# Kernel optimization log

Measured on AMD Instinct MI355X. Metric: run time of the kernel, lower is better.

Reference implementation:

```python
import jax, jax.numpy as jnp
import numpy as np
from jax import lax

B, S, TW = 16, 128, 16
VOCAB, EDIM = 50000, 300
NCHARS, CEDIM, CH = 100, 50, 50
HID = 256
NTAGS, MAXR = 10, 16
H2 = 2 * HID


def _lstm_dir(x, mask, wih, whh, b):
    # x: [N,T,D], mask: [N,T] bool. Returns masked outputs [N,T,H] and final hidden [N,H].
    Hd = whh.shape[1]
    Nn = x.shape[0]

    def step(carry, inp):
        h, c = carry
        xt, m = inp  # xt [N,D], m [N,1]
        z = xt @ wih.T + h @ whh.T + b
        i, f, g, o = jnp.split(z, 4, axis=-1)
        c_new = jax.nn.sigmoid(f) * c + jax.nn.sigmoid(i) * jnp.tanh(g)
        h_new = jax.nn.sigmoid(o) * jnp.tanh(c_new)
        c = jnp.where(m, c_new, c)
        h = jnp.where(m, h_new, h)
        return (h, c), jnp.where(m, h_new, 0.0)

    h0 = jnp.zeros((Nn, Hd), x.dtype)
    (hn, _), ys = lax.scan(step, (h0, h0), (x.transpose(1, 0, 2), mask.T[..., None]))
    return ys.transpose(1, 0, 2), hn


def _bilstm(x, lengths, pf, pb):
    # Mirrors pack_padded_sequence -> LSTM -> pad_packed (zeros past length).
    T = x.shape[1]
    mask = jnp.arange(T)[None, :] < lengths[:, None]
    yf, hf = _lstm_dir(x, mask, *pf)
    # per-sequence reversal for the backward direction
    idx = jnp.maximum(lengths[:, None] - 1 - jnp.arange(T)[None, :], 0)
    xr = jnp.take_along_axis(x, idx[:, :, None], axis=1)
    ybr, hb = _lstm_dir(xr, mask, *pb)
    yb = jnp.take_along_axis(ybr, idx[:, :, None], axis=1) * mask[:, :, None]
    return jnp.concatenate([yf, yb], -1), jnp.concatenate([hf, hb], -1)


def _forward(emb, char_emb, c_wih_f, c_whh_f, c_b_f, c_wih_b, c_whh_b, c_b_b,
             w_wih_f, w_whh_f, w_b_f, w_wih_b, w_whh_b, w_b_b, clf_w, clf_b,
             sentences, sentence_lengths, word_chars, word_lengths):
    word_repr = emb[sentences]  # [B,S,EDIM]
    # CharLSTM: final bi-hidden per word (all words of all sentences batched)
    cw = word_chars.reshape(B * S, TW)
    cl = word_lengths.reshape(B * S)
    ce = char_emb[cw]  # [B*S,TW,CEDIM]
    _, hn = _bilstm(ce, cl, (c_wih_f, c_whh_f, c_b_f), (c_wih_b, c_whh_b, c_b_b))
    sent_mask = jnp.arange(S)[None, :] < sentence_lengths[:, None]
    char_feat = hn.reshape(B, S, 2 * CH) * sent_mask[:, :, None]  # pad_sequence zeros
    x = jnp.concatenate([word_repr, char_feat], -1)  # [B,S,400]
    out, _ = _bilstm(x, sentence_lengths, (w_wih_f, w_whh_f, w_b_f), (w_wih_b, w_whh_b, w_b_b))
    u = out.transpose(1, 0, 2)  # [S,B,2H]  (unpacked.transpose(0,1))
    # prefix sums collapse the exhaustive sliding-window means into one pass
    csum = jnp.concatenate([jnp.zeros((1, B, H2), u.dtype), jnp.cumsum(u, axis=0)], 0)
    starts = np.concatenate([np.arange(0, S - r + 1) for r in range(1, MAXR + 1)])
    sizes = np.concatenate([np.full(S - r + 1, r) for r in range(1, MAXR + 1)])
    first = u[starts]                                   # [N,B,2H]
    last = u[starts + sizes - 1]                        # [N,B,2H]
    mean = (csum[starts + sizes] - csum[starts]) / jnp.asarray(sizes, u.dtype)[:, None, None]
    feats = jnp.concatenate([first, mean, last], -1)    # [N,B,6H]
    logits = jax.nn.relu(feats) @ clf_w.T + clf_b       # [N,B,NTAGS]
    return logits.transpose(1, 2, 0)                    # [B,NTAGS,N] (stack dim=-1)


def setup_inputs() -> dict:
    key = jax.random.key(0)
    ks = jax.random.split(key, 12)
    sc = 0.08

    def lstm_p(k, D, Hd):
        k1, k2, k3 = jax.random.split(k, 3)
        return (jax.random.normal(k1, (4 * Hd, D), jnp.float32) * sc,
                jax.random.normal(k2, (4 * Hd, Hd), jnp.float32) * sc,
                jax.random.normal(k3, (4 * Hd,), jnp.float32) * sc)

    emb = (jax.random.normal(ks[0], (VOCAB, EDIM), jnp.float32) * sc).at[0].set(0.0)
    char_emb = (jax.random.normal(ks[1], (NCHARS, CEDIM), jnp.float32) * sc).at[0].set(0.0)
    c_wih_f, c_whh_f, c_b_f = lstm_p(ks[2], CEDIM, CH)
    c_wih_b, c_whh_b, c_b_b = lstm_p(ks[3], CEDIM, CH)
    w_wih_f, w_whh_f, w_b_f = lstm_p(ks[4], EDIM + 2 * CH, HID)
    w_wih_b, w_whh_b, w_b_b = lstm_p(ks[5], EDIM + 2 * CH, HID)
    clf_w = jax.random.normal(ks[6], (NTAGS, 3 * H2), jnp.float32) * sc
    clf_b = jax.random.normal(ks[7], (NTAGS,), jnp.float32) * sc

    sentences = jax.random.randint(ks[8], (B, S), 1, VOCAB, jnp.int32)
    sl = jnp.sort(jax.random.randint(ks[9], (B,), S // 2, S + 1, jnp.int32))[::-1]
    sentence_lengths = sl.at[0].set(S)  # descending; max_len = S (static)
    word_chars = jax.random.randint(ks[10], (B, S, TW), 1, NCHARS, jnp.int32)
    word_lengths = jax.random.randint(ks[11], (B, S), 1, TW + 1, jnp.int32)

    return dict(emb=emb, char_emb=char_emb,
                c_wih_f=c_wih_f, c_whh_f=c_whh_f, c_b_f=c_b_f,
                c_wih_b=c_wih_b, c_whh_b=c_whh_b, c_b_b=c_b_b,
                w_wih_f=w_wih_f, w_whh_f=w_whh_f, w_b_f=w_b_f,
                w_wih_b=w_wih_b, w_whh_b=w_whh_b, w_b_b=w_b_b,
                clf_w=clf_w, clf_b=clf_b,
                sentences=sentences, sentence_lengths=sentence_lengths,
                word_chars=word_chars, word_lengths=word_lengths)


def reference(emb, char_emb, c_wih_f, c_whh_f, c_b_f, c_wih_b, c_whh_b, c_b_b,
              w_wih_f, w_whh_f, w_b_f, w_wih_b, w_whh_b, w_b_b, clf_w, clf_b,
              sentences, sentence_lengths, word_chars, word_lengths):
    return _forward(emb, char_emb, c_wih_f, c_whh_f, c_b_f, c_wih_b, c_whh_b, c_b_b,
                    w_wih_f, w_whh_f, w_b_f, w_wih_b, w_whh_b, w_b_b, clf_w, clf_b,
                    sentences, sentence_lengths, word_chars, word_lengths)
```

## Files before the change

kernel.cpp:

```cpp
#include <hip/hip_runtime.h>
#include <math.h>

typedef unsigned int u32;
typedef unsigned short u16;
typedef __attribute__((ext_vector_type(8))) short short8;
typedef __attribute__((ext_vector_type(4))) float f32x4;
typedef __attribute__((ext_vector_type(4))) u32 u32x4;

#define NB 16
#define NS 128
#define NTW 16
#define NEDIM 300
#define NCED 50
#define NCH 50
#define NTAGS 10
#define XDIM 400
#define NWIN 1928

__device__ __forceinline__ float sigf(float x){ return 1.0f/(1.0f+__expf(-x)); }
__device__ __forceinline__ float tanhfast(float x){
  float e = __expf(2.0f*x);
  return 1.0f - 2.0f/(e + 1.0f);
}
__device__ __forceinline__ u16 f2bu(float f){
  u32 u = __float_as_uint(f);
  return (u16)((u + 0x7fffu + ((u>>16)&1u))>>16);
}
__device__ __forceinline__ float bf2f(u16 x){ return __uint_as_float(((u32)x)<<16); }

__global__ void k_embed(const float* __restrict__ emb, const int* __restrict__ sent,
                        float* __restrict__ x){
  int n = blockIdx.x;
  int row = sent[n];
  const float* src = emb + (size_t)row*NEDIM;
  float* dst = x + (size_t)n*XDIM;
  for (int d = threadIdx.x; d < NEDIM; d += blockDim.x) dst[d] = src[d];
}

__global__ void k_char(const float* __restrict__ char_emb,
                       const float* __restrict__ wih_f, const float* __restrict__ whh_f, const float* __restrict__ b_f,
                       const float* __restrict__ wih_b, const float* __restrict__ whh_b, const float* __restrict__ b_b,
                       const int* __restrict__ wchars, const int* __restrict__ wlens,
                       const int* __restrict__ slens, float* __restrict__ x){
  const int dir = blockIdx.y;
  const int tid = threadIdx.x;
  __shared__ u16 wih_l[200*NCED];
  __shared__ u16 whh_l[200*NCED];
  __shared__ float z_l[200];
  __shared__ float h_l[NCH];
  const float* wih = dir ? wih_b : wih_f;
  const float* whh = dir ? whh_b : whh_f;
  const float* bp  = dir ? b_b   : b_f;
  for (int i = tid; i < 200*NCED; i += 256){
    wih_l[i] = f2bu(wih[i]);
    whh_l[i] = f2bu(whh[i]);
  }
  float bias = (tid < 200) ? bp[tid] : 0.f;
  __syncthreads();
  for (int w = 0; w < 4; ++w){
    int n = blockIdx.x*4 + w;
    int b = n >> 7, s = n & 127;
    int len = wlens[n];
    float c = 0.f, hcur = 0.f;
    if (tid < NCH) h_l[tid] = 0.f;
    __syncthreads();
    for (int t = 0; t < len; ++t){
      int tt = dir ? (len-1-t) : t;
      int ch = wchars[n*NTW + tt];
      if (tid < 200){
        const float* xe = char_emb + ch*NCED;
        const u16* wr = wih_l + tid*NCED;
        const u16* ur = whh_l + tid*NCED;
        float acc = bias;
        #pragma unroll 10
        for (int k = 0; k < NCED; ++k){
          float wv = __uint_as_float(((u32)wr[k])<<16);
          float uv = __uint_as_float(((u32)ur[k])<<16);
          acc += wv*xe[k] + uv*h_l[k];
        }
        z_l[tid] = acc;
      }
      __syncthreads();
      if (tid < NCH){
        float gi = sigf(z_l[tid]);
        float gf = sigf(z_l[NCH+tid]);
        float gg = tanhf(z_l[2*NCH+tid]);
        float go = sigf(z_l[3*NCH+tid]);
        c = gf*c + gi*gg;
        hcur = go*tanhf(c);
        h_l[tid] = hcur;
      }
      __syncthreads();
    }
    if (tid < NCH){
      float v = (s < slens[b]) ? hcur : 0.f;
      x[(size_t)n*XDIM + NEDIM + dir*NCH + tid] = v;
    }
  }
}

__global__ void k_wxg(const float* __restrict__ x,
                      const float* __restrict__ wih_f, const float* __restrict__ wih_b,
                      const float* __restrict__ bw_f, const float* __restrict__ bw_b,
                      u16* __restrict__ xgb){
  __shared__ float As[16][65];
  __shared__ float Bs[16][65];
  int tid = threadIdx.x;
  int tx = tid & 15, ty = tid >> 4;
  int n0 = blockIdx.x * 64;
  int m0 = blockIdx.y * 64;
  int dir = n0 >> 10;
  int j0  = n0 & 1023;
  const float* wih = dir ? wih_b : wih_f;
  const float* bw  = dir ? bw_b  : bw_f;
  float acc[4][4] = {};
  for (int k0 = 0; k0 < 400; k0 += 16){
    #pragma unroll
    for (int i = 0; i < 4; ++i){
      int e = tid + i*256;
      int kk = e & 15, m = e >> 4;
      As[kk][m] = x[(m0+m)*XDIM + k0 + kk];
      Bs[kk][m] = wih[(j0+m)*XDIM + k0 + kk];
    }
    __syncthreads();
    #pragma unroll
    for (int kk = 0; kk < 16; ++kk){
      float av[4], bv[4];
      #pragma unroll
      for (int i=0;i<4;++i) av[i] = As[kk][ty*4+i];
      #pragma unroll
      for (int j=0;j<4;++j) bv[j] = Bs[kk][tx*4+j];
      #pragma unroll
      for (int i=0;i<4;++i)
        #pragma unroll
        for (int j=0;j<4;++j) acc[i][j] = fmaf(av[i], bv[j], acc[i][j]);
    }
    __syncthreads();
  }
  #pragma unroll
  for (int i=0;i<4;++i){
    int m = m0 + ty*4 + i;
    #pragma unroll
    for (int j=0;j<4;++j){
      int jj = j0 + tx*4 + j;
      xgb[(size_t)dir*2097152 + m*1024 + jj] = f2bu(acc[i][j] + bw[jj]);
    }
  }
}

__global__ __launch_bounds__(1024, 4) void k_wlstm2(
    const float* __restrict__ whh_f, const float* __restrict__ whh_b,
    const u16* __restrict__ xgB, const int* __restrict__ slens,
    float* __restrict__ out, u32* __restrict__ xh, int* __restrict__ flags){
  const int dir  = blockIdx.x >> 1;
  const int half = blockIdx.x & 1;
  const int tid  = threadIdx.x;
  const int lane = tid & 63;
  const int w    = tid >> 6;
  const int q    = lane >> 4;
  const int jc   = lane & 15;

  __shared__ __align__(16) u16  Hbuf[2][16*256];
  __shared__ __align__(16) float abuf[32][64][4];
  __shared__ __align__(16) u16  xstg[2][16*512];

  const float* whh = dir ? whh_b : whh_f;

  const int v = w & 7, rsel = w >> 3;
  const int b0c = q*4 + 2*rsel, b1c = b0c + 1;
  const int len0 = slens[b0c], len1 = slens[b1c];
  const int len_s = slens[w];

  short8 Bf[2][8];
  #pragma unroll
  for (int l = 0; l < 2; ++l){
    int jt = w*2 + l;
    int g = jt >> 3, vv = jt & 7;
    int j = g*256 + half*128 + vv*16 + jc;
    const float* wr = whh + (size_t)j*256;
    #pragma unroll
    for (int kc = 0; kc < 8; ++kc){
      int k0 = kc*32 + q*8;
      f32x4 w0 = *(const f32x4*)(wr + k0);
      f32x4 w1 = *(const f32x4*)(wr + k0 + 4);
      short8 s;
      s[0]=(short)f2bu(w0[0]); s[1]=(short)f2bu(w0[1]);
      s[2]=(short)f2bu(w0[2]); s[3]=(short)f2bu(w0[3]);
      s[4]=(short)f2bu(w1[0]); s[5]=(short)f2bu(w1[1]);
      s[6]=(short)f2bu(w1[2]); s[7]=(short)f2bu(w1[3]);
      Bf[l][kc] = s;
    }
  }

  for (int i = tid; i < 2048; i += 1024) ((u32*)Hbuf[0])[i] = 0u;

  {
    int rowS = dir ? (len_s - 1) : 0;
    const u16* src = xgB + ((size_t)dir<<21) + ((w*128 + rowS)*1024 + q*256 + half*128 + jc*8);
    u32x4 d = *(const u32x4*)src;
    *(u32x4*)&xstg[0][(w*4 + q)*128 + jc*8] = d;
  }
  __syncthreads();

  const int fl_idx = dir*2 + half;
  const int fl_p   = dir*2 + (1 - half);
  u32* xh_own = xh + fl_idx*2048;
  u32* xh_par = xh + fl_p*2048;

  float c0 = 0.f, c1 = 0.f, h0 = 0.f, h1 = 0.f;
  int cur = 0;

  for (int t = 0; t < 128; ++t){
    u32x4 stg;
    const bool do_stage = (t < 127);
    if (do_stage){
      int rowS = dir ? (len_s - 2 - t) : (t + 1);
      rowS = rowS < 0 ? 0 : rowS;
      const u16* src = xgB + ((size_t)dir<<21) + ((w*128 + rowS)*1024 + q*256 + half*128 + jc*8);
      stg = *(const u32x4*)src;
    }

    f32x4 acc0 = {0.f,0.f,0.f,0.f};
    f32x4 acc1 = {0.f,0.f,0.f,0.f};
    {
      const char* Hc = (const char*)Hbuf[cur];
      int arow = jc;
      #pragma unroll
      for (int kc = 0; kc < 8; ++kc){
        int kb = (kc*64 + q*16) ^ ((arow & 7) << 4);
        short8 af = *(const short8*)(Hc + arow*512 + kb);
        acc0 = __builtin_amdgcn_mfma_f32_16x16x32_bf16(af, Bf[0][kc], acc0, 0, 0, 0);
        acc1 = __builtin_amdgcn_mfma_f32_16x16x32_bf16(af, Bf[1][kc], acc1, 0, 0, 0);
      }
    }
    *(f32x4*)&abuf[w*2  ][lane][0] = acc0;
    *(f32x4*)&abuf[w*2+1][lane][0] = acc1;
    __syncthreads();

    int nxt = cur ^ 1;
    {
      f32x4 zi = *(const f32x4*)&abuf[0*8+v][lane][0];
      f32x4 zf = *(const f32x4*)&abuf[1*8+v][lane][0];
      f32x4 zg = *(const f32x4*)&abuf[2*8+v][lane][0];
      f32x4 zo = *(const f32x4*)&abuf[3*8+v][lane][0];
      const u16* xs = xstg[t & 1];
      const int ucol = v*16 + jc;
      const int ug   = half*128 + ucol;

      float Zi0 = (rsel ? zi[2] : zi[0]) + bf2f(xs[(b0c*4+0)*128 + ucol]);
      float Zf0 = (rsel ? zf[2] : zf[0]) + bf2f(xs[(b0c*4+1)*128 + ucol]);
      float Zg0 = (rsel ? zg[2] : zg[0]) + bf2f(xs[(b0c*4+2)*128 + ucol]);
      float Zo0 = (rsel ? zo[2] : zo[0]) + bf2f(xs[(b0c*4+3)*128 + ucol]);
      if (t < len0){
        float gi = sigf(Zi0), gf = sigf(Zf0), gg = tanhfast(Zg0), go = sigf(Zo0);
        c0 = gf*c0 + gi*gg;
        h0 = go*tanhfast(c0);
        int row = dir ? (len0-1-t) : t;
        out[((b0c<<7)+row)*512 + dir*256 + ug] = h0;
      }
      float Zi1 = (rsel ? zi[3] : zi[1]) + bf2f(xs[(b1c*4+0)*128 + ucol]);
      float Zf1 = (rsel ? zf[3] : zf[1]) + bf2f(xs[(b1c*4+1)*128 + ucol]);
      float Zg1 = (rsel ? zg[3] : zg[1]) + bf2f(xs[(b1c*4+2)*128 + ucol]);
      float Zo1 = (rsel ? zo[3] : zo[1]) + bf2f(xs[(b1c*4+3)*128 + ucol]);
      if (t < len1){
        float gi = sigf(Zi1), gf = sigf(Zf1), gg = tanhfast(Zg1), go = sigf(Zo1);
        c1 = gf*c1 + gi*gg;
        h1 = go*tanhfast(c1);
        int row = dir ? (len1-1-t) : t;
        out[((b1c<<7)+row)*512 + dir*256 + ug] = h1;
      }
      u16 hb0 = f2bu(h0), hb1 = f2bu(h1);
      Hbuf[nxt][b0c*256 + ((((ug*2) ^ ((b0c&7)<<4))) >> 1)] = hb0;
      Hbuf[nxt][b1c*256 + ((((ug*2) ^ ((b1c&7)<<4))) >> 1)] = hb1;
      u32 pack = ((u32)hb1 << 16) | (u32)hb0;
      __hip_atomic_store(&xh_own[(t&1)*1024 + ucol*8 + q*2 + rsel], pack,
                         __ATOMIC_RELAXED, __HIP_MEMORY_SCOPE_AGENT);
    }
    __syncthreads();

    if (tid == 0){
      __hip_atomic_store(&flags[fl_idx], t+1, __ATOMIC_RELEASE, __HIP_MEMORY_SCOPE_AGENT);
      int spins = 0;
      while (__hip_atomic_load(&flags[fl_p], __ATOMIC_ACQUIRE, __HIP_MEMORY_SCOPE_AGENT) < t+1){
        __builtin_amdgcn_s_sleep(2);
        if (++spins > (1<<16)) break;
      }
    }
    __syncthreads();

    {
      u32 d = __hip_atomic_load(&xh_par[(t&1)*1024 + tid],
                                __ATOMIC_RELAXED, __HIP_MEMORY_SCOPE_AGENT);
      int ul  = tid >> 3;
      int qq  = (tid >> 1) & 3, rs = tid & 1;
      int bb0 = qq*4 + rs*2, bb1 = bb0 + 1;
      int ugp = (1-half)*128 + ul;
      Hbuf[nxt][bb0*256 + ((((ugp*2) ^ ((bb0&7)<<4))) >> 1)] = (u16)(d & 0xffffu);
      Hbuf[nxt][bb1*256 + ((((ugp*2) ^ ((bb1&7)<<4))) >> 1)] = (u16)(d >> 16);
    }
    if (do_stage){
      *(u32x4*)&xstg[(t+1)&1][(w*4 + q)*128 + jc*8] = stg;
    }
    __syncthreads();
    cur = nxt;
  }
}

__global__ void k_csum(const float* __restrict__ out, float* __restrict__ csum){
  int gid = blockIdx.x*256 + threadIdx.x;
  int b = gid >> 9, d = gid & 511;
  float run = 0.f;
  csum[(b*129)*512 + d] = 0.f;
  for (int s = 0; s < 128; ++s){
    run += out[((b<<7)+s)*512 + d];
    csum[(b*129 + s + 1)*512 + d] = run;
  }
}

__global__ void k_ac(const float* __restrict__ out, const float* __restrict__ clf_w,
                     float* __restrict__ A, float* __restrict__ Cm){
  int gid = blockIdx.x*256 + threadIdx.x;
  int bs = gid / 10, tag = gid % 10;
  const float* o  = out + bs*512;
  const float* w1 = clf_w + tag*1536;
  const float* w3 = w1 + 1024;
  float a=0.f, cc=0.f;
  for (int d = 0; d < 512; ++d){
    float vv = fmaxf(o[d], 0.f);
    a  = fmaf(vv, w1[d], a);
    cc = fmaf(vv, w3[d], cc);
  }
  A[gid] = a; Cm[gid] = cc;
}

__global__ void k_clf(const float* __restrict__ csum, const float* __restrict__ clf_w,
                      const float* __restrict__ clf_b, const float* __restrict__ A,
                      const float* __restrict__ Cm, float* __restrict__ dout){
  __shared__ float w2_l[NTAGS*512];
  int tid = threadIdx.x;
  for (int i = tid; i < NTAGS*512; i += 256){
    int tag = i >> 9, d = i & 511;
    w2_l[i] = clf_w[tag*1536 + 512 + d];
  }
  __syncthreads();
  int qq = blockIdx.x*4 + (tid >> 6);
  int lane = tid & 63;
  int n = qq >> 4, b = qq & 15;
  int rem = n, r = 1;
  while (rem >= 129 - r){ rem -= 129 - r; ++r; }
  int s0 = rem, s1 = s0 + r - 1;
  float invr = 1.0f / (float)r;
  int d0 = lane*8;
  const float* c0 = csum + (b*129 + s0    )*512 + d0;
  const float* c1 = csum + (b*129 + s0 + r)*512 + d0;
  float m[8];
  #pragma unroll
  for (int i=0;i<8;++i) m[i] = fmaxf((c1[i]-c0[i])*invr, 0.f);
  float p[10];
  #pragma unroll
  for (int tag=0; tag<NTAGS; ++tag){
    const float* wv = w2_l + tag*512 + d0;
    float s = 0.f;
    #pragma unroll
    for (int i=0;i<8;++i) s = fmaf(m[i], wv[i], s);
    #pragma unroll
    for (int off=32; off>=1; off>>=1) s += __shfl_xor(s, off);
    p[tag] = s;
  }
  if (lane == 0){
    #pragma unroll
    for (int tag=0; tag<NTAGS; ++tag){
      float vv = p[tag] + A[(b*128+s0)*10+tag] + Cm[(b*128+s1)*10+tag] + clf_b[tag];
      dout[b*(NTAGS*NWIN) + tag*NWIN + n] = vv;
    }
  }
}

extern "C" void kernel_launch(void* const* d_in, const int* in_sizes, int n_in,
                              void* d_out, int out_size, void* d_ws, size_t ws_size,
                              hipStream_t stream){
  (void)in_sizes; (void)n_in; (void)out_size; (void)ws_size;
  const float* emb      = (const float*)d_in[0];
  const float* char_emb = (const float*)d_in[1];
  const float* c_wih_f  = (const float*)d_in[2];
  const float* c_whh_f  = (const float*)d_in[3];
  const float* c_b_f    = (const float*)d_in[4];
  const float* c_wih_b  = (const float*)d_in[5];
  const float* c_whh_b  = (const float*)d_in[6];
  const float* c_b_b    = (const float*)d_in[7];
  const float* w_wih_f  = (const float*)d_in[8];
  const float* w_whh_f  = (const float*)d_in[9];
  const float* w_b_f    = (const float*)d_in[10];
  const float* w_wih_b  = (const float*)d_in[11];
  const float* w_whh_b  = (const float*)d_in[12];
  const float* w_b_b    = (const float*)d_in[13];
  const float* clf_w    = (const float*)d_in[14];
  const float* clf_b    = (const float*)d_in[15];
  const int* sentences  = (const int*)d_in[16];
  const int* slens      = (const int*)d_in[17];
  const int* wchars     = (const int*)d_in[18];
  const int* wlens      = (const int*)d_in[19];

  float* ws   = (float*)d_ws;
  float* x    = ws;
  u16*  xgb   = (u16*)(ws + 819200);
  float* outb = ws + 2916352;
  float* csum = ws + 3964928;
  float* A    = ws + 5021696;
  float* Cm   = ws + 5042176;
  u32*  xh    = (u32*)(ws + 5062656);
  int*  flags = (int*)(ws + 5070848);

  hipMemsetAsync(outb, 0, (size_t)2048*512*sizeof(float), stream);
  hipMemsetAsync(flags, 0, 256, stream);
  k_embed<<<2048, 256, 0, stream>>>(emb, sentences, x);
  k_char<<<dim3(512,2), 256, 0, stream>>>(char_emb, c_wih_f, c_whh_f, c_b_f,
                                          c_wih_b, c_whh_b, c_b_b,
                                          wchars, wlens, slens, x);
  k_wxg<<<dim3(32,32), 256, 0, stream>>>(x, w_wih_f, w_wih_b, w_b_f, w_b_b, xgb);
  k_wlstm2<<<4, 1024, 0, stream>>>(w_whh_f, w_whh_b, xgb, slens, outb, xh, flags);
  k_csum<<<32, 256, 0, stream>>>(outb, csum);
  k_ac<<<80, 256, 0, stream>>>(outb, clf_w, A, Cm);
  k_clf<<<7712, 256, 0, stream>>>(csum, clf_w, clf_b, A, Cm, (float*)d_out);
}
```

Measured before the change: 899.3 us.

## Run each word-LSTM direction in one block, removing cross-block flag sync

The word-level recurrent kernel now uses a single 512-thread block per direction instead of two cooperating 1024-thread blocks. Those blocks exchanged half of the hidden state through global atomics and spin flags every timestep; that exchange is gone. Recurrent weights are split between registers (first 6 k-tiles) and LDS (last 2), and the input-gate projection is written by the GEMM kernel in a time-major layout already permuted per thread, so each step does four contiguous vector loads. The cost is twice the MFMA work per block and fewer threads per direction on the serial critical path.

```diff
diff --git a/kernel.cpp b/kernel.cpp
--- a/kernel.cpp
+++ b/kernel.cpp
@@ -102,7 +102,8 @@
 __global__ void k_wxg(const float* __restrict__ x,
                       const float* __restrict__ wih_f, const float* __restrict__ wih_b,
                       const float* __restrict__ bw_f, const float* __restrict__ bw_b,
-                      u16* __restrict__ xgb){
+                      const int* __restrict__ slens,
+                      u16* __restrict__ xgT){
   __shared__ float As[16][65];
   __shared__ float Bs[16][65];
   int tid = threadIdx.x;
@@ -137,169 +138,157 @@
     }
     __syncthreads();
   }
+  int b_ = m0 >> 7;
+  int len = slens[b_];
+  int q_ = b_ >> 2, r_ = b_ & 3;
   #pragma unroll
   for (int i=0;i<4;++i){
     int m = m0 + ty*4 + i;
-    #pragma unroll
-    for (int j=0;j<4;++j){
-      int jj = j0 + tx*4 + j;
-      xgb[(size_t)dir*2097152 + m*1024 + jj] = f2bu(acc[i][j] + bw[jj]);
-    }
-  }
-}
-
-__global__ __launch_bounds__(1024, 4) void k_wlstm2(
+    int row = m & 127;
+    int t = dir ? (len-1-row) : row;
+    if (t >= 0){
+      #pragma unroll
+      for (int j=0;j<4;++j){
+        int jj = j0 + tx*4 + j;
+        float v = acc[i][j] + bw[jj];
+        int g = jj >> 8, u = jj & 255;
+        int ut = u >> 4, jc_ = u & 15;
+        int w_ = ut >> 1, u2_ = ut & 1;
+        int p_ = g & 1, gg_ = g >> 1;
+        int tid_ = w_*64 + q_*16 + jc_;
+        size_t e = ((size_t)((dir<<7) + t)*512 + tid_)*32 + p_*16 + gg_*8 + u2_*4 + r_;
+        xgT[e] = f2bu(v);
+      }
+    }
+  }
+}
+
+__global__ __launch_bounds__(512, 2) void k_wlstm3(
     const float* __restrict__ whh_f, const float* __restrict__ whh_b,
-    const u16* __restrict__ xgB, const int* __restrict__ slens,
-    float* __restrict__ out, u32* __restrict__ xh, int* __restrict__ flags){
-  const int dir  = blockIdx.x >> 1;
-  const int half = blockIdx.x & 1;
+    const u16* __restrict__ xgT, const int* __restrict__ slens,
+    float* __restrict__ out){
+  const int dir  = blockIdx.x;
   const int tid  = threadIdx.x;
   const int lane = tid & 63;
   const int w    = tid >> 6;
   const int q    = lane >> 4;
   const int jc   = lane & 15;
 
-  __shared__ __align__(16) u16  Hbuf[2][16*256];
-  __shared__ __align__(16) float abuf[32][64][4];
-  __shared__ __align__(16) u16  xstg[2][16*512];
+  __shared__ __align__(16) u32 WL[2][64][64][4];
+  __shared__ __align__(16) u16 Hs[2][16][256];
 
   const float* whh = dir ? whh_b : whh_f;
 
-  const int v = w & 7, rsel = w >> 3;
-  const int b0c = q*4 + 2*rsel, b1c = b0c + 1;
-  const int len0 = slens[b0c], len1 = slens[b1c];
-  const int len_s = slens[w];
-
-  short8 Bf[2][8];
+  int lenr[4];
   #pragma unroll
-  for (int l = 0; l < 2; ++l){
-    int jt = w*2 + l;
-    int g = jt >> 3, vv = jt & 7;
-    int j = g*256 + half*128 + vv*16 + jc;
-    const float* wr = whh + (size_t)j*256;
-    #pragma unroll
-    for (int kc = 0; kc < 8; ++kc){
-      int k0 = kc*32 + q*8;
-      f32x4 w0 = *(const f32x4*)(wr + k0);
-      f32x4 w1 = *(const f32x4*)(wr + k0 + 4);
-      short8 s;
-      s[0]=(short)f2bu(w0[0]); s[1]=(short)f2bu(w0[1]);
-      s[2]=(short)f2bu(w0[2]); s[3]=(short)f2bu(w0[3]);
-      s[4]=(short)f2bu(w1[0]); s[5]=(short)f2bu(w1[1]);
-      s[6]=(short)f2bu(w1[2]); s[7]=(short)f2bu(w1[3]);
-      Bf[l][kc] = s;
-    }
-  }
-
-  for (int i = tid; i < 2048; i += 1024) ((u32*)Hbuf[0])[i] = 0u;
-
-  {
-    int rowS = dir ? (len_s - 1) : 0;
-    const u16* src = xgB + ((size_t)dir<<21) + ((w*128 + rowS)*1024 + q*256 + half*128 + jc*8);
-    u32x4 d = *(const u32x4*)src;
-    *(u32x4*)&xstg[0][(w*4 + q)*128 + jc*8] = d;
-  }
+  for (int r=0;r<4;++r) lenr[r] = slens[q*4+r];
+
+  short8 Wf[4][2][6];
+  #pragma unroll
+  for (int g=0; g<4; ++g){
+    #pragma unroll
+    for (int u2=0; u2<2; ++u2){
+      int j = g*256 + (2*w+u2)*16 + jc;
+      const float* wr = whh + (size_t)j*256;
+      #pragma unroll
+      for (int kt=0; kt<6; ++kt){
+        int k0 = kt*32 + q*8;
+        f32x4 w0 = *(const f32x4*)(wr + k0);
+        f32x4 w1 = *(const f32x4*)(wr + k0 + 4);
+        short8 s;
+        s[0]=(short)f2bu(w0[0]); s[1]=(short)f2bu(w0[1]);
+        s[2]=(short)f2bu(w0[2]); s[3]=(short)f2bu(w0[3]);
+        s[4]=(short)f2bu(w1[0]); s[5]=(short)f2bu(w1[1]);
+        s[6]=(short)f2bu(w1[2]); s[7]=(short)f2bu(w1[3]);
+        Wf[g][u2][kt] = s;
+      }
+    }
+  }
+
+  for (int idx = tid; idx < 2*64*64; idx += 512){
+    int kt2 = idx >> 12; int rem = idx & 4095;
+    int jt = rem >> 6;   int ln = rem & 63;
+    int g = jt >> 4, ut = jt & 15;
+    int j = g*256 + ut*16 + (ln & 15);
+    int k0 = (6+kt2)*32 + (ln>>4)*8;
+    const float* wr = whh + (size_t)j*256 + k0;
+    f32x4 w0 = *(const f32x4*)(wr);
+    f32x4 w1 = *(const f32x4*)(wr + 4);
+    WL[kt2][jt][ln][0] = ((u32)f2bu(w0[1])<<16) | f2bu(w0[0]);
+    WL[kt2][jt][ln][1] = ((u32)f2bu(w0[3])<<16) | f2bu(w0[2]);
+    WL[kt2][jt][ln][2] = ((u32)f2bu(w1[1])<<16) | f2bu(w1[0]);
+    WL[kt2][jt][ln][3] = ((u32)f2bu(w1[3])<<16) | f2bu(w1[2]);
+  }
+
+  for (int i = tid; i < 2048; i += 512) ((u32*)Hs[0])[i] = 0u;
   __syncthreads();
 
-  const int fl_idx = dir*2 + half;
-  const int fl_p   = dir*2 + (1 - half);
-  u32* xh_own = xh + fl_idx*2048;
-  u32* xh_par = xh + fl_p*2048;
-
-  float c0 = 0.f, c1 = 0.f, h0 = 0.f, h1 = 0.f;
+  float c[2][4] = {{0.f,0.f,0.f,0.f},{0.f,0.f,0.f,0.f}};
+  float P[2][4];
+  const u16* xbase = xgT + ((size_t)(dir*128)*512 + tid)*32;
   int cur = 0;
 
   for (int t = 0; t < 128; ++t){
-    u32x4 stg;
-    const bool do_stage = (t < 127);
-    if (do_stage){
-      int rowS = dir ? (len_s - 2 - t) : (t + 1);
-      rowS = rowS < 0 ? 0 : rowS;
-      const u16* src = xgB + ((size_t)dir<<21) + ((w*128 + rowS)*1024 + q*256 + half*128 + jc*8);
-      stg = *(const u32x4*)src;
-    }
-
-    f32x4 acc0 = {0.f,0.f,0.f,0.f};
-    f32x4 acc1 = {0.f,0.f,0.f,0.f};
-    {
-      const char* Hc = (const char*)Hbuf[cur];
-      int arow = jc;
-      #pragma unroll
-      for (int kc = 0; kc < 8; ++kc){
-        int kb = (kc*64 + q*16) ^ ((arow & 7) << 4);
-        short8 af = *(const short8*)(Hc + arow*512 + kb);
-        acc0 = __builtin_amdgcn_mfma_f32_16x16x32_bf16(af, Bf[0][kc], acc0, 0, 0, 0);
-        acc1 = __builtin_amdgcn_mfma_f32_16x16x32_bf16(af, Bf[1][kc], acc1, 0, 0, 0);
-      }
-    }
-    *(f32x4*)&abuf[w*2  ][lane][0] = acc0;
-    *(f32x4*)&abuf[w*2+1][lane][0] = acc1;
-    __syncthreads();
-
+    const u16* xp = xbase + (size_t)t*16384;
+    u32x4 xv[4];
+    #pragma unroll
+    for (int i=0;i<4;++i) xv[i] = *(const u32x4*)(xp + i*8);
+
+    const char* Hc = (const char*)Hs[cur];
     int nxt = cur ^ 1;
-    {
-      f32x4 zi = *(const f32x4*)&abuf[0*8+v][lane][0];
-      f32x4 zf = *(const f32x4*)&abuf[1*8+v][lane][0];
-      f32x4 zg = *(const f32x4*)&abuf[2*8+v][lane][0];
-      f32x4 zo = *(const f32x4*)&abuf[3*8+v][lane][0];
-      const u16* xs = xstg[t & 1];
-      const int ucol = v*16 + jc;
-      const int ug   = half*128 + ucol;
-
-      float Zi0 = (rsel ? zi[2] : zi[0]) + bf2f(xs[(b0c*4+0)*128 + ucol]);
-      float Zf0 = (rsel ? zf[2] : zf[0]) + bf2f(xs[(b0c*4+1)*128 + ucol]);
-      float Zg0 = (rsel ? zg[2] : zg[0]) + bf2f(xs[(b0c*4+2)*128 + ucol]);
-      float Zo0 = (rsel ? zo[2] : zo[0]) + bf2f(xs[(b0c*4+3)*128 + ucol]);
-      if (t < len0){
-        float gi = sigf(Zi0), gf = sigf(Zf0), gg = tanhfast(Zg0), go = sigf(Zo0);
-        c0 = gf*c0 + gi*gg;
-        h0 = go*tanhfast(c0);
-        int row = dir ? (len0-1-t) : t;
-        out[((b0c<<7)+row)*512 + dir*256 + ug] = h0;
-      }
-      float Zi1 = (rsel ? zi[3] : zi[1]) + bf2f(xs[(b1c*4+0)*128 + ucol]);
-      float Zf1 = (rsel ? zf[3] : zf[1]) + bf2f(xs[(b1c*4+1)*128 + ucol]);
-      float Zg1 = (rsel ? zg[3] : zg[1]) + bf2f(xs[(b1c*4+2)*128 + ucol]);
-      float Zo1 = (rsel ? zo[3] : zo[1]) + bf2f(xs[(b1c*4+3)*128 + ucol]);
-      if (t < len1){
-        float gi = sigf(Zi1), gf = sigf(Zf1), gg = tanhfast(Zg1), go = sigf(Zo1);
-        c1 = gf*c1 + gi*gg;
-        h1 = go*tanhfast(c1);
-        int row = dir ? (len1-1-t) : t;
-        out[((b1c<<7)+row)*512 + dir*256 + ug] = h1;
-      }
-      u16 hb0 = f2bu(h0), hb1 = f2bu(h1);
-      Hbuf[nxt][b0c*256 + ((((ug*2) ^ ((b0c&7)<<4))) >> 1)] = hb0;
-      Hbuf[nxt][b1c*256 + ((((ug*2) ^ ((b1c&7)<<4))) >> 1)] = hb1;
-      u32 pack = ((u32)hb1 << 16) | (u32)hb0;
-      __hip_atomic_store(&xh_own[(t&1)*1024 + ucol*8 + q*2 + rsel], pack,
-                         __ATOMIC_RELAXED, __HIP_MEMORY_SCOPE_AGENT);
-    }
-    __syncthreads();
-
-    if (tid == 0){
-      __hip_atomic_store(&flags[fl_idx], t+1, __ATOMIC_RELEASE, __HIP_MEMORY_SCOPE_AGENT);
-      int spins = 0;
-      while (__hip_atomic_load(&flags[fl_p], __ATOMIC_ACQUIRE, __HIP_MEMORY_SCOPE_AGENT) < t+1){
-        __builtin_amdgcn_s_sleep(2);
-        if (++spins > (1<<16)) break;
-      }
-    }
-    __syncthreads();
-
-    {
-      u32 d = __hip_atomic_load(&xh_par[(t&1)*1024 + tid],
-                                __ATOMIC_RELAXED, __HIP_MEMORY_SCOPE_AGENT);
-      int ul  = tid >> 3;
-      int qq  = (tid >> 1) & 3, rs = tid & 1;
-      int bb0 = qq*4 + rs*2, bb1 = bb0 + 1;
-      int ugp = (1-half)*128 + ul;
-      Hbuf[nxt][bb0*256 + ((((ugp*2) ^ ((bb0&7)<<4))) >> 1)] = (u16)(d & 0xffffu);
-      Hbuf[nxt][bb1*256 + ((((ugp*2) ^ ((bb1&7)<<4))) >> 1)] = (u16)(d >> 16);
-    }
-    if (do_stage){
-      *(u32x4*)&xstg[(t+1)&1][(w*4 + q)*128 + jc*8] = stg;
+    u16* Hn = (u16*)Hs[nxt];
+
+    #pragma unroll
+    for (int p = 0; p < 2; ++p){
+      f32x4 a[2][2] = {{{0.f,0.f,0.f,0.f},{0.f,0.f,0.f,0.f}},
+                       {{0.f,0.f,0.f,0.f},{0.f,0.f,0.f,0.f}}};
+      #pragma unroll
+      for (int kt = 0; kt < 8; ++kt){
+        short8 af = *(const short8*)(Hc + jc*512 + ((kt*64 + q*16) ^ ((jc&7)<<4)));
+        if (kt < 6){
+          #pragma unroll
+          for (int gg=0; gg<2; ++gg){
+            #pragma unroll
+            for (int u2=0; u2<2; ++u2)
+              a[gg][u2] = __builtin_amdgcn_mfma_f32_16x16x32_bf16(af, Wf[gg*2+p][u2][kt], a[gg][u2], 0,0,0);
+          }
+        } else {
+          #pragma unroll
+          for (int gg=0; gg<2; ++gg){
+            #pragma unroll
+            for (int u2=0; u2<2; ++u2){
+              short8 wl = *(const short8*)&WL[kt-6][(gg*2+p)*16 + 2*w+u2][lane][0];
+              a[gg][u2] = __builtin_amdgcn_mfma_f32_16x16x32_bf16(af, wl, a[gg][u2], 0,0,0);
+            }
+          }
+        }
+      }
+      #pragma unroll
+      for (int u2=0; u2<2; ++u2){
+        #pragma unroll
+        for (int r=0; r<4; ++r){
+          float x0 = bf2f((u16)(xv[p*2+0][(u2*4+r)>>1] >> (((u2*4+r)&1)*16)));
+          float x1 = bf2f((u16)(xv[p*2+1][(u2*4+r)>>1] >> (((u2*4+r)&1)*16)));
+          if (p == 0){
+            float zi = a[0][u2][r] + x0;
+            float zg = a[1][u2][r] + x1;
+            P[u2][r] = sigf(zi) * tanhfast(zg);
+          } else {
+            float zf = a[0][u2][r] + x0;
+            float zo = a[1][u2][r] + x1;
+            float cc = sigf(zf)*c[u2][r] + P[u2][r];
+            c[u2][r] = cc;
+            float h = sigf(zo)*tanhfast(cc);
+            int b_ = q*4 + r;
+            int u_ = (2*w+u2)*16 + jc;
+            Hn[b_*256 + (((u_*2) ^ ((b_&7)<<4))>>1)] = f2bu(h);
+            if (t < lenr[r]){
+              int row = dir ? (lenr[r]-1-t) : t;
+              out[((b_<<7)+row)*512 + dir*256 + u_] = h;
+            }
+          }
+        }
+      }
     }
     __syncthreads();
     cur = nxt;
@@ -403,22 +392,19 @@
 
   float* ws   = (float*)d_ws;
   float* x    = ws;
-  u16*  xgb   = (u16*)(ws + 819200);
+  u16*  xgT   = (u16*)(ws + 819200);
   float* outb = ws + 2916352;
   float* csum = ws + 3964928;
   float* A    = ws + 5021696;
   float* Cm   = ws + 5042176;
-  u32*  xh    = (u32*)(ws + 5062656);
-  int*  flags = (int*)(ws + 5070848);
 
   hipMemsetAsync(outb, 0, (size_t)2048*512*sizeof(float), stream);
-  hipMemsetAsync(flags, 0, 256, stream);
   k_embed<<<2048, 256, 0, stream>>>(emb, sentences, x);
   k_char<<<dim3(512,2), 256, 0, stream>>>(char_emb, c_wih_f, c_whh_f, c_b_f,
                                           c_wih_b, c_whh_b, c_b_b,
                                           wchars, wlens, slens, x);
-  k_wxg<<<dim3(32,32), 256, 0, stream>>>(x, w_wih_f, w_wih_b, w_b_f, w_b_b, xgb);
-  k_wlstm2<<<4, 1024, 0, stream>>>(w_whh_f, w_whh_b, xgb, slens, outb, xh, flags);
+  k_wxg<<<dim3(32,32), 256, 0, stream>>>(x, w_wih_f, w_wih_b, w_b_f, w_b_b, slens, xgT);
+  k_wlstm3<<<2, 512, 0, stream>>>(w_whh_f, w_whh_b, xgT, slens, outb);
   k_csum<<<32, 256, 0, stream>>>(outb, csum);
   k_ac<<<80, 256, 0, stream>>>(outb, clf_w, A, Cm);
   k_clf<<<7712, 256, 0, stream>>>(csum, clf_w, clf_b, A, Cm, (float*)d_out);
```

After: 1.182 ms. +31.4%, slower.
